# Performance work log

Measured on AMD Instinct MI355X. Metric: run time of the kernel, lower is better.

## Reference

```python
import jax, jax.numpy as jnp
import numpy as np
import math

B, S, D = 4, 2048, 1024

def setup_inputs() -> dict:
    key = jax.random.key(0)
    k1, k2, k3, k4 = jax.random.split(key, 4)
    scale = 1.0 / math.sqrt(D)
    return {
        "x": jax.random.normal(k1, (B, S, D), dtype=jnp.float32),
        "w_q": jax.random.normal(k2, (D, D), dtype=jnp.float32) * scale,
        "w_k": jax.random.normal(k3, (D, D), dtype=jnp.float32) * scale,
        "w_v": jax.random.normal(k4, (D, D), dtype=jnp.float32) * scale,
        "causal": 1,
    }

def reference(x, w_q, w_k, w_v, causal):
    # QKV projections: nn.Linear(dim, dim, bias=False) -> x @ W.T
    q = jnp.einsum('bsd,ed->bse', x, w_q)
    k = jnp.einsum('bsd,ed->bse', x, w_k)
    v = jnp.einsum('bsd,ed->bse', x, w_v)
    d_k = q.shape[-1]
    scores = jnp.einsum('bqd,bkd->bqk', q, k) / jnp.sqrt(jnp.asarray(d_k, q.dtype))
    if causal:
        seq_len = q.shape[-2]
        mask = jnp.triu(jnp.ones((seq_len, seq_len), dtype=bool), k=1)
        scores = jnp.where(mask, jnp.asarray(-jnp.inf, scores.dtype), scores)
    weights = jax.nn.softmax(scores, axis=-1)
    return jnp.einsum('bqk,bkd->bqd', weights, v)
```

## Files before the change

kernel.cpp:

```cpp
#include <hip/hip_runtime.h>
#include <stdint.h>

typedef unsigned short u16;
typedef __attribute__((ext_vector_type(8))) __bf16 bf16x8;
typedef __attribute__((ext_vector_type(4))) float f32x4;

__device__ __forceinline__ u16 f2bf(float f) {
  unsigned u = __float_as_uint(f);
  u += 0x7FFF + ((u >> 16) & 1);
  return (u16)(u >> 16);
}

__device__ __forceinline__ float bf2f(u16 h) {
  return __uint_as_float(((unsigned)h) << 16);
}

__device__ __forceinline__ void llds16(const u16* g, u16* l) {
  __builtin_amdgcn_global_load_lds(
      (const __attribute__((address_space(1))) void*)g,
      (__attribute__((address_space(3))) void*)l, 16, 0, 0);
}

__global__ __launch_bounds__(256) void cast_all(
    const float* __restrict__ x, const float* __restrict__ wq,
    const float* __restrict__ wk, const float* __restrict__ wv,
    u16* __restrict__ xb, u16* __restrict__ wb, float* __restrict__ lsum) {
  int i = blockIdx.x * 256 + threadIdx.x;
  if (i < 8192) lsum[i] = 0.f;
  const float* src; u16* dst; int off;
  if (i < 2097152)      { src = x;  dst = xb;            off = i; }
  else if (i < 2359296) { src = wq; dst = wb;            off = i - 2097152; }
  else if (i < 2621440) { src = wk; dst = wb + 1048576;  off = i - 2359296; }
  else                  { src = wv; dst = wb + 2097152;  off = i - 2621440; }
  float4 f = ((const float4*)src)[off];
  ushort4 o;
  o.x = f2bf(f.x); o.y = f2bf(f.y); o.z = f2bf(f.z); o.w = f2bf(f.w);
  ((ushort4*)dst)[off] = o;
}

template<int MODE>
__global__ __launch_bounds__(256) void gemm_nt(
    const u16* __restrict__ A, long long sA, int lda,
    const u16* __restrict__ B, long long sB, int ldb,
    void* __restrict__ Cp, long long sC, int ldc,
    int K, u16* __restrict__ vt, float scale,
    float* __restrict__ lsum, const int* __restrict__ causalp) {
  const int t = threadIdx.x;
  const int causal = (MODE == 0) ? 1 : causalp[0];

  int rt = blockIdx.x, ct = blockIdx.y;
  if (MODE == 1) {
    int x = blockIdx.x;
    if (x < 136) {
      int r = (int)((sqrtf(8.0f * x + 1.0f) - 1.0f) * 0.5f);
      while ((r + 1) * (r + 2) / 2 <= x) ++r;
      while (r * (r + 1) / 2 > x) --r;
      rt = r; ct = x - r * (r + 1) / 2;
    } else {
      int y = x - 136;
      int r = (int)((sqrtf(8.0f * y + 1.0f) - 1.0f) * 0.5f);
      while ((r + 1) * (r + 2) / 2 <= y) ++r;
      while (r * (r + 1) / 2 > y) --r;
      int c = y - r * (r + 1) / 2;
      rt = c; ct = r + 1;
      if (causal) return;
    }
  }
  if (MODE == 2) rt = 15 - blockIdx.x;

  const int rowbase = rt * 128;
  const int colbase = ct * 128;
  const u16* Ab = A + (long long)blockIdx.z * sA;
  const u16* Bb = B + (long long)blockIdx.z * sB;

  int Keff = K;
  if (MODE == 2 && causal) Keff = min(K, rowbase + 128);

  __shared__ u16 As[8192];
  __shared__ u16 Bs[8192];

  const int lane = t & 63;
  const int wv = t >> 6;
  const int wr = wv >> 1;
  const int wc = wv & 1;
  const int quad = lane >> 4;
  const int lr = lane & 15;

  f32x4 acc[4][4];
  const f32x4 zero = {0.f, 0.f, 0.f, 0.f};
#pragma unroll
  for (int i = 0; i < 4; ++i)
#pragma unroll
    for (int j = 0; j < 4; ++j) acc[i][j] = zero;

  {
    const int csw = (t & 7) ^ ((t >> 3) & 7);
    const u16* ga = Ab + (long long)(rowbase + (t >> 3)) * lda + csw * 8;
    const u16* gb = Bb + (long long)(colbase + (t >> 3)) * ldb + csw * 8;
    const long long ra = 32LL * lda, rb = 32LL * ldb;
    u16* la = As + t * 8;
    u16* lb = Bs + t * 8;

    const int m7 = lr & 7;
    const int a_base = (wr * 64 + lr) * 64 + ((quad ^ m7) * 8);
    const int b_base = (wc * 64 + lr) * 64 + ((quad ^ m7) * 8);

    for (int k0 = 0; k0 < Keff; k0 += 64) {
      __syncthreads();
#pragma unroll
      for (int i = 0; i < 4; ++i) {
        llds16(ga + k0 + i * ra, la + i * 2048);
        llds16(gb + k0 + i * rb, lb + i * 2048);
      }
      __syncthreads();
#pragma unroll
      for (int ks = 0; ks < 2; ++ks) {
        const int ko = ks ? 32 : 0;
        bf16x8 af[4], bfv[4];
#pragma unroll
        for (int tm = 0; tm < 4; ++tm)
          af[tm] = *(const bf16x8*)(As + ((a_base + tm * 1024) ^ ko));
#pragma unroll
        for (int tn = 0; tn < 4; ++tn)
          bfv[tn] = *(const bf16x8*)(Bs + ((b_base + tn * 1024) ^ ko));
#pragma unroll
        for (int tm = 0; tm < 4; ++tm)
#pragma unroll
          for (int tn = 0; tn < 4; ++tn)
            acc[tm][tn] = __builtin_amdgcn_mfma_f32_16x16x32_bf16(
                af[tm], bfv[tn], acc[tm][tn], 0, 0, 0);
      }
    }
  }

  if (MODE == 0 && colbase >= 2048) {
#pragma unroll
    for (int tm = 0; tm < 4; ++tm) {
      int s0 = rowbase + wr * 64 + tm * 16 + quad * 4;
      int b = s0 >> 11;
      int sl = s0 & 2047;
#pragma unroll
      for (int tn = 0; tn < 4; ++tn) {
        int e = colbase - 2048 + wc * 64 + tn * 16 + lr;
        ushort4 o;
        o.x = f2bf(acc[tm][tn][0]);
        o.y = f2bf(acc[tm][tn][1]);
        o.z = f2bf(acc[tm][tn][2]);
        o.w = f2bf(acc[tm][tn][3]);
        *(ushort4*)(vt + ((long long)(b * 1024 + e)) * 2048 + sl) = o;
      }
    }
    return;
  }

#pragma unroll
  for (int tm = 0; tm < 4; ++tm) {
#pragma unroll
    for (int r = 0; r < 4; ++r) {
      const int grow = rowbase + wr * 64 + tm * 16 + quad * 4 + r;
      float li, rsum = 0.f;
      if (MODE == 2) li = __builtin_amdgcn_rcpf(lsum[blockIdx.z * 2048 + grow]);
#pragma unroll
      for (int tn = 0; tn < 4; ++tn) {
        const int gcol = colbase + wc * 64 + tn * 16 + lr;
        float val = acc[tm][tn][r];
        if (MODE == 0) {
          ((u16*)Cp)[(long long)grow * ldc + gcol] = f2bf(val);
        } else if (MODE == 1) {
          u16* C = (u16*)Cp + (long long)blockIdx.z * sC;
          float ex = (causal && gcol > grow) ? 0.f : __expf(val * scale);
          C[(long long)grow * ldc + gcol] = f2bf(ex);
          rsum += ex;
        } else {
          float* C = (float*)Cp + (long long)blockIdx.z * sC;
          C[(long long)grow * ldc + gcol] = val * li;
        }
      }
      if (MODE == 1) {
#pragma unroll
        for (int o = 8; o > 0; o >>= 1) rsum += __shfl_xor(rsum, o, 64);
        if (lr == 0)
          atomicAdd(&lsum[blockIdx.z * 2048 + grow], rsum);
      }
    }
  }
}

extern "C" void kernel_launch(void* const* d_in, const int* in_sizes, int n_in,
                              void* d_out, int out_size, void* d_ws, size_t ws_size,
                              hipStream_t stream) {
  const float* x  = (const float*)d_in[0];
  const float* wq = (const float*)d_in[1];
  const float* wk = (const float*)d_in[2];
  const float* wv = (const float*)d_in[3];
  const int* causal = (const int*)d_in[4];
  float* out = (float*)d_out;

  char* ws = (char*)d_ws;
  u16* xb = (u16*)(ws);
  u16* wb = (u16*)(ws + 16777216);
  u16* qk = (u16*)(ws + 23068672);
  u16* vt = (u16*)(ws + 56623104);
  u16* sb = (u16*)(ws + 73400320);
  float* lsum = (float*)(ws + 106954752);

  cast_all<<<11264, 256, 0, stream>>>(x, wq, wk, wv, xb, wb, lsum);

  gemm_nt<0><<<dim3(64, 24, 1), 256, 0, stream>>>(
      xb, 0, 1024, wb, 0, 1024, qk, 0, 2048, 1024, vt, 1.0f, nullptr, causal);

  gemm_nt<1><<<dim3(256, 1, 4), 256, 0, stream>>>(
      qk, 2048LL * 2048, 2048, qk + 1024, 2048LL * 2048, 2048,
      sb, 2048LL * 2048, 2048, 1024, nullptr, 0.03125f, lsum, causal);

  gemm_nt<2><<<dim3(16, 8, 4), 256, 0, stream>>>(
      sb, 2048LL * 2048, 2048, vt, 1024LL * 2048, 2048,
      out, 2048LL * 1024, 1024, 2048, nullptr, 1.0f, lsum, causal);
}
```

Baseline: 235.8 us.

## Split attention GEMMs into 64x128 tile kernel with finer causal triangle mapping

The QKV projection becomes its own kernel, and the score and PV GEMMs move to a new kernel that uses 64x128 tiles with each of the four waves owning a 32-column strip. The causal score grid is remapped over 64-row by 128-column tiles, so fewer fully masked elements are computed and the diagonal waste is smaller. The PV kernel's K range is clipped to rowbase+64. Doubling the block count is meant to improve CU occupancy and load balance on the triangular work. The cost is lower MFMA reuse per LDS load, since each wave now issues 8 MFMAs per k-step instead of 16.

```diff
diff --git a/kernel.cpp b/kernel.cpp
--- a/kernel.cpp
+++ b/kernel.cpp
@@ -38,43 +38,13 @@
   ((ushort4*)dst)[off] = o;
 }
 
-template<int MODE>
-__global__ __launch_bounds__(256) void gemm_nt(
-    const u16* __restrict__ A, long long sA, int lda,
-    const u16* __restrict__ B, long long sB, int ldb,
-    void* __restrict__ Cp, long long sC, int ldc,
-    int K, u16* __restrict__ vt, float scale,
-    float* __restrict__ lsum, const int* __restrict__ causalp) {
+__global__ __launch_bounds__(256) void gemm_qkv(
+    const u16* __restrict__ A, int lda,
+    const u16* __restrict__ B, int ldb,
+    u16* __restrict__ C, int ldc, int K, u16* __restrict__ vt) {
   const int t = threadIdx.x;
-  const int causal = (MODE == 0) ? 1 : causalp[0];
-
-  int rt = blockIdx.x, ct = blockIdx.y;
-  if (MODE == 1) {
-    int x = blockIdx.x;
-    if (x < 136) {
-      int r = (int)((sqrtf(8.0f * x + 1.0f) - 1.0f) * 0.5f);
-      while ((r + 1) * (r + 2) / 2 <= x) ++r;
-      while (r * (r + 1) / 2 > x) --r;
-      rt = r; ct = x - r * (r + 1) / 2;
-    } else {
-      int y = x - 136;
-      int r = (int)((sqrtf(8.0f * y + 1.0f) - 1.0f) * 0.5f);
-      while ((r + 1) * (r + 2) / 2 <= y) ++r;
-      while (r * (r + 1) / 2 > y) --r;
-      int c = y - r * (r + 1) / 2;
-      rt = c; ct = r + 1;
-      if (causal) return;
-    }
-  }
-  if (MODE == 2) rt = 15 - blockIdx.x;
-
-  const int rowbase = rt * 128;
-  const int colbase = ct * 128;
-  const u16* Ab = A + (long long)blockIdx.z * sA;
-  const u16* Bb = B + (long long)blockIdx.z * sB;
-
-  int Keff = K;
-  if (MODE == 2 && causal) Keff = min(K, rowbase + 128);
+  const int rowbase = blockIdx.x * 128;
+  const int colbase = blockIdx.y * 128;
 
   __shared__ u16 As[8192];
   __shared__ u16 Bs[8192];
@@ -95,8 +65,8 @@
 
   {
     const int csw = (t & 7) ^ ((t >> 3) & 7);
-    const u16* ga = Ab + (long long)(rowbase + (t >> 3)) * lda + csw * 8;
-    const u16* gb = Bb + (long long)(colbase + (t >> 3)) * ldb + csw * 8;
+    const u16* ga = A + (long long)(rowbase + (t >> 3)) * lda + csw * 8;
+    const u16* gb = B + (long long)(colbase + (t >> 3)) * ldb + csw * 8;
     const long long ra = 32LL * lda, rb = 32LL * ldb;
     u16* la = As + t * 8;
     u16* lb = Bs + t * 8;
@@ -105,7 +75,7 @@
     const int a_base = (wr * 64 + lr) * 64 + ((quad ^ m7) * 8);
     const int b_base = (wc * 64 + lr) * 64 + ((quad ^ m7) * 8);
 
-    for (int k0 = 0; k0 < Keff; k0 += 64) {
+    for (int k0 = 0; k0 < K; k0 += 64) {
       __syncthreads();
 #pragma unroll
       for (int i = 0; i < 4; ++i) {
@@ -133,7 +103,7 @@
     }
   }
 
-  if (MODE == 0 && colbase >= 2048) {
+  if (colbase >= 2048) {
 #pragma unroll
     for (int tm = 0; tm < 4; ++tm) {
       int s0 = rowbase + wr * 64 + tm * 16 + quad * 4;
@@ -154,19 +124,123 @@
   }
 
 #pragma unroll
-  for (int tm = 0; tm < 4; ++tm) {
+  for (int tm = 0; tm < 4; ++tm)
 #pragma unroll
     for (int r = 0; r < 4; ++r) {
       const int grow = rowbase + wr * 64 + tm * 16 + quad * 4 + r;
+#pragma unroll
+      for (int tn = 0; tn < 4; ++tn) {
+        const int gcol = colbase + wc * 64 + tn * 16 + lr;
+        C[(long long)grow * ldc + gcol] = f2bf(acc[tm][tn][r]);
+      }
+    }
+}
+
+template<int MODE>
+__global__ __launch_bounds__(256) void gemm_att(
+    const u16* __restrict__ A, long long sA, int lda,
+    const u16* __restrict__ B, long long sB, int ldb,
+    void* __restrict__ Cp, long long sC, int ldc,
+    int K, float scale, float* __restrict__ lsum,
+    const int* __restrict__ causalp) {
+  const int t = threadIdx.x;
+  const int causal = causalp[0];
+
+  int rt, ct;
+  if (MODE == 1) {
+    int x = blockIdx.x;
+    if (causal) {
+      if (x >= 272) return;
+      int p = (int)((sqrtf(4.0f * x + 1.0f) - 1.0f) * 0.5f);
+      while ((p + 1) * (p + 2) <= x) ++p;
+      while (p * (p + 1) > x) --p;
+      int rem = x - p * (p + 1);
+      int hi = (rem >= p + 1) ? 1 : 0;
+      rt = 2 * p + hi;
+      ct = rem - hi * (p + 1);
+    } else {
+      rt = x >> 4; ct = x & 15;
+    }
+  } else {
+    rt = 31 - blockIdx.x;
+    ct = blockIdx.y;
+  }
+
+  const int rowbase = rt * 64;
+  const int colbase = ct * 128;
+  const u16* Ab = A + (long long)blockIdx.z * sA;
+  const u16* Bb = B + (long long)blockIdx.z * sB;
+
+  int Keff = K;
+  if (MODE == 2 && causal) Keff = min(K, rowbase + 64);
+
+  __shared__ u16 As[4096];
+  __shared__ u16 Bs[8192];
+
+  const int lane = t & 63;
+  const int w = t >> 6;
+  const int quad = lane >> 4;
+  const int lr = lane & 15;
+
+  f32x4 acc[4][2];
+  const f32x4 zero = {0.f, 0.f, 0.f, 0.f};
+#pragma unroll
+  for (int i = 0; i < 4; ++i)
+#pragma unroll
+    for (int j = 0; j < 2; ++j) acc[i][j] = zero;
+
+  {
+    const int csw = (t & 7) ^ ((t >> 3) & 7);
+    const u16* ga = Ab + (long long)(rowbase + (t >> 3)) * lda + csw * 8;
+    const u16* gb = Bb + (long long)(colbase + (t >> 3)) * ldb + csw * 8;
+    const long long ra = 32LL * lda, rb = 32LL * ldb;
+    u16* la = As + t * 8;
+    u16* lb = Bs + t * 8;
+
+    const int m7 = lr & 7;
+    const int a_base = lr * 64 + ((quad ^ m7) * 8);
+    const int b_base = (w * 32 + lr) * 64 + ((quad ^ m7) * 8);
+
+    for (int k0 = 0; k0 < Keff; k0 += 64) {
+      __syncthreads();
+      llds16(ga + k0, la);
+      llds16(ga + k0 + ra, la + 2048);
+#pragma unroll
+      for (int i = 0; i < 4; ++i)
+        llds16(gb + k0 + i * rb, lb + i * 2048);
+      __syncthreads();
+#pragma unroll
+      for (int ks = 0; ks < 2; ++ks) {
+        const int ko = ks ? 32 : 0;
+        bf16x8 af[4], bfv[2];
+#pragma unroll
+        for (int tm = 0; tm < 4; ++tm)
+          af[tm] = *(const bf16x8*)(As + ((a_base + tm * 1024) ^ ko));
+#pragma unroll
+        for (int tn = 0; tn < 2; ++tn)
+          bfv[tn] = *(const bf16x8*)(Bs + ((b_base + tn * 1024) ^ ko));
+#pragma unroll
+        for (int tm = 0; tm < 4; ++tm)
+#pragma unroll
+          for (int tn = 0; tn < 2; ++tn)
+            acc[tm][tn] = __builtin_amdgcn_mfma_f32_16x16x32_bf16(
+                af[tm], bfv[tn], acc[tm][tn], 0, 0, 0);
+      }
+    }
+  }
+
+#pragma unroll
+  for (int tm = 0; tm < 4; ++tm)
+#pragma unroll
+    for (int r = 0; r < 4; ++r) {
+      const int grow = rowbase + tm * 16 + quad * 4 + r;
       float li, rsum = 0.f;
       if (MODE == 2) li = __builtin_amdgcn_rcpf(lsum[blockIdx.z * 2048 + grow]);
 #pragma unroll
-      for (int tn = 0; tn < 4; ++tn) {
-        const int gcol = colbase + wc * 64 + tn * 16 + lr;
+      for (int tn = 0; tn < 2; ++tn) {
+        const int gcol = colbase + w * 32 + tn * 16 + lr;
         float val = acc[tm][tn][r];
-        if (MODE == 0) {
-          ((u16*)Cp)[(long long)grow * ldc + gcol] = f2bf(val);
-        } else if (MODE == 1) {
+        if (MODE == 1) {
           u16* C = (u16*)Cp + (long long)blockIdx.z * sC;
           float ex = (causal && gcol > grow) ? 0.f : __expf(val * scale);
           C[(long long)grow * ldc + gcol] = f2bf(ex);
@@ -183,7 +257,6 @@
           atomicAdd(&lsum[blockIdx.z * 2048 + grow], rsum);
       }
     }
-  }
 }
 
 extern "C" void kernel_launch(void* const* d_in, const int* in_sizes, int n_in,
@@ -206,14 +279,14 @@
 
   cast_all<<<11264, 256, 0, stream>>>(x, wq, wk, wv, xb, wb, lsum);
 
-  gemm_nt<0><<<dim3(64, 24, 1), 256, 0, stream>>>(
-      xb, 0, 1024, wb, 0, 1024, qk, 0, 2048, 1024, vt, 1.0f, nullptr, causal);
-
-  gemm_nt<1><<<dim3(256, 1, 4), 256, 0, stream>>>(
+  gemm_qkv<<<dim3(64, 24), 256, 0, stream>>>(
+      xb, 1024, wb, 1024, qk, 2048, 1024, vt);
+
+  gemm_att<1><<<dim3(512, 1, 4), 256, 0, stream>>>(
       qk, 2048LL * 2048, 2048, qk + 1024, 2048LL * 2048, 2048,
-      sb, 2048LL * 2048, 2048, 1024, nullptr, 0.03125f, lsum, causal);
-
-  gemm_nt<2><<<dim3(16, 8, 4), 256, 0, stream>>>(
+      sb, 2048LL * 2048, 2048, 1024, 0.03125f, lsum, causal);
+
+  gemm_att<2><<<dim3(32, 8, 4), 256, 0, stream>>>(
       sb, 2048LL * 2048, 2048, vt, 1024LL * 2048, 2048,
-      out, 2048LL * 1024, 1024, 2048, nullptr, 1.0f, lsum, causal);
-}
+      out, 2048LL * 1024, 1024, 2048, 1.0f, lsum, causal);
+}
```

Result: slower. 241.6 us (+2.5%).
